# Optimization experiments

Hardware: AMD Instinct MI355X
Metric: run time of the kernel (lower is better)

Reference implementation:

```python
import jax, jax.numpy as jnp
import numpy as np

STRIDE = 4
H, W, A = 208, 336, 3
ANCHOR_SCALE = 8.0
ASPECTS = ((1.0, 1.0), (1.4, 0.7), (0.7, 1.4))  # (aspect_x, aspect_y)
PRE_NMS = 2000
POST_NMS = 1000
IOU_THR = 0.7
BBOX_CLIP = float(np.log(1000.0 / 16.0))


def make_anchors():
    # EfficientDet/SageMakerCV-style anchors at level 2, boxes as (y1, x1, y2, x2)
    base = ANCHOR_SCALE * STRIDE  # 32
    yc = (np.arange(H, dtype=np.float32) + 0.5) * STRIDE
    xc = (np.arange(W, dtype=np.float32) + 0.5) * STRIDE
    yy, xx = np.meshgrid(yc, xc, indexing='ij')  # [H, W]
    per_aspect = []
    for ax, ay in ASPECTS:
        hx, hy = base * ax / 2.0, base * ay / 2.0
        per_aspect.append(np.stack([yy - hy, xx - hx, yy + hy, xx + hx], axis=-1))
    return np.stack(per_aspect, axis=2).reshape(-1, 4).astype(np.float32)  # [H*W*A, 4]


def decode(deltas, anchors):
    # deltas: [B, N, 4] (dy, dx, dh, dw); anchors: [N, 4]; weights (1,1,1,1)
    ah = anchors[:, 2] - anchors[:, 0]
    aw = anchors[:, 3] - anchors[:, 1]
    acy = anchors[:, 0] + 0.5 * ah
    acx = anchors[:, 1] + 0.5 * aw
    dy, dx = deltas[..., 0], deltas[..., 1]
    dh = jnp.clip(deltas[..., 2], -BBOX_CLIP, BBOX_CLIP)
    dw = jnp.clip(deltas[..., 3], -BBOX_CLIP, BBOX_CLIP)
    cy = dy * ah + acy
    cx = dx * aw + acx
    h = jnp.exp(dh) * ah
    w = jnp.exp(dw) * aw
    return jnp.stack([cy - 0.5 * h, cx - 0.5 * w, cy + 0.5 * h, cx + 0.5 * w], axis=-1)


def _iou_one_to_many(box, boxes):
    y1 = jnp.maximum(box[0], boxes[:, 0])
    x1 = jnp.maximum(box[1], boxes[:, 1])
    y2 = jnp.minimum(box[2], boxes[:, 2])
    x2 = jnp.minimum(box[3], boxes[:, 3])
    inter = jnp.maximum(y2 - y1, 0.0) * jnp.maximum(x2 - x1, 0.0)
    a1 = (box[2] - box[0]) * (box[3] - box[1])
    a2 = (boxes[:, 2] - boxes[:, 0]) * (boxes[:, 3] - boxes[:, 1])
    return inter / (a1 + a2 - inter + 1e-8)


def nms_single(boxes, scores):
    # greedy NMS, fixed POST_NMS iterations (jit-friendly)
    def body(i, state):
        sc, kb, ks = state
        j = jnp.argmax(sc)
        b, s = boxes[j], sc[j]
        kb = kb.at[i].set(b)
        ks = ks.at[i].set(s)
        sup = _iou_one_to_many(b, boxes) > IOU_THR  # suppresses j itself (iou=1)
        sc = jnp.where(sup, -1.0, sc)
        return sc, kb, ks

    init = (scores,
            jnp.zeros((POST_NMS, 4), boxes.dtype),
            jnp.zeros((POST_NMS,), scores.dtype))
    _, kb, ks = jax.lax.fori_loop(0, POST_NMS, body, init)
    return kb, ks


def setup_inputs() -> dict:
    key = jax.random.key(0)
    k0, k1, k2 = jax.random.split(key, 3)
    feats = jax.random.normal(k0, (2, H, W, 256), dtype=jnp.float32)
    img_info = jnp.ones((2, 2), jnp.float32) * jnp.array([832.0, 1344.0], jnp.float32)
    w_cls = 0.01 * jax.random.normal(k1, (256, A * 1), dtype=jnp.float32)
    b_cls = jnp.zeros((A * 1,), jnp.float32)
    w_reg = 0.01 * jax.random.normal(k2, (256, A * 4), dtype=jnp.float32)
    b_reg = jnp.zeros((A * 4,), jnp.float32)
    return {"feats": feats, "img_info": img_info, "w_cls": w_cls, "b_cls": b_cls,
            "w_reg": w_reg, "b_reg": b_reg}


def reference(feats, img_info, w_cls, b_cls, w_reg, b_reg):
    B = feats.shape[0]
    # 1x1 convs == channel matmuls
    cls_scores = jnp.einsum('bhwc,co->bhwo', feats, w_cls) + b_cls  # [B,H,W,3]
    bbox_preds = jnp.einsum('bhwc,co->bhwo', feats, w_reg) + b_reg  # [B,H,W,12]

    scores = jax.nn.sigmoid(cls_scores).reshape(B, -1)       # [B, N]
    deltas = bbox_preds.reshape(B, -1, 4)                    # [B, N, 4]
    anchors = jnp.asarray(make_anchors())                    # [N, 4]
    boxes = decode(deltas, anchors)                          # [B, N, 4]

    # clip to image extents
    hmax = img_info[:, 0][:, None]
    wmax = img_info[:, 1][:, None]
    boxes = jnp.stack([
        jnp.clip(boxes[..., 0], 0.0, hmax),
        jnp.clip(boxes[..., 1], 0.0, wmax),
        jnp.clip(boxes[..., 2], 0.0, hmax),
        jnp.clip(boxes[..., 3], 0.0, wmax)], axis=-1)

    # per-image pre-NMS topk
    top_s, idx = jax.lax.top_k(scores, PRE_NMS)              # [B, PRE]
    top_b = jnp.take_along_axis(boxes, idx[..., None], axis=1)  # [B, PRE, 4]

    rois, roi_scores = jax.vmap(nms_single)(top_b, top_s)    # [B, POST, 4], [B, POST]
    return cls_scores, bbox_preds, rois, roi_scores
```

## Files before the change

### kernel.cpp

```cpp
#include <hip/hip_runtime.h>
#include <cstdint>
#include <cstddef>

#define HH 208
#define WW 336
#define NA 3
#define NPER 209664
#define NROWS 139776
#define NB 2
#define PRE_K 2000
#define POST_K 1000
#define CAP 8192
#define MW 32
#define MROWS 2048
#define BBOX_CLIP_F 4.135166556742356f

#define WS_HIST   0
#define WS_HIST2  32768
#define WS_META   65536
#define WS_META24 65544
#define WS_CCNT   65552
#define WS_KEEPW  65568
#define WS_CAND   66080
#define WS_SBOX   197152
#define WS_SSC    261152
#define WS_MASK   277248
#define WS_ZERO_WORDS 49288

__device__ __forceinline__ float sigmoidf_ref(float x) {
  return __fdiv_rn(1.0f, __fadd_rn(1.0f, expf(-x)));
}
__device__ __forceinline__ unsigned int score_u(float logit) {
  float s = sigmoidf_ref(logit);
  return __float_as_uint(s) | 0x80000000u;
}

__device__ __forceinline__ unsigned long long bcast64(unsigned long long v, int l) {
  unsigned int lo = (unsigned int)__builtin_amdgcn_readlane((int)(unsigned int)v, l);
  unsigned int hi = (unsigned int)__builtin_amdgcn_readlane((int)(unsigned int)(v >> 32), l);
  return ((unsigned long long)hi << 32) | lo;
}

__device__ __forceinline__ float4 decode_box(const float* __restrict__ bbox,
                                             int b, unsigned int n,
                                             float hmax, float wmax) {
  unsigned int a = n % 3u;
  unsigned int pix = n / 3u;
  unsigned int y = pix / (unsigned int)WW;
  unsigned int x = pix % (unsigned int)WW;
  float yc = ((float)y + 0.5f) * 4.0f;
  float xc = ((float)x + 0.5f) * 4.0f;
  float hx = (a == 0) ? 16.0f : ((a == 1) ? 22.4f : 11.2f);
  float hy = (a == 0) ? 16.0f : ((a == 1) ? 11.2f : 22.4f);
  float ay1 = __fsub_rn(yc, hy), ax1 = __fsub_rn(xc, hx);
  float ay2 = __fadd_rn(yc, hy), ax2 = __fadd_rn(xc, hx);
  float ah = __fsub_rn(ay2, ay1), aw = __fsub_rn(ax2, ax1);
  float acy = __fadd_rn(ay1, __fmul_rn(0.5f, ah));
  float acx = __fadd_rn(ax1, __fmul_rn(0.5f, aw));
  const float* d = bbox + ((size_t)b * NPER + n) * 4u;
  float dy = d[0], dx = d[1];
  float dh = fminf(fmaxf(d[2], -BBOX_CLIP_F), BBOX_CLIP_F);
  float dw = fminf(fmaxf(d[3], -BBOX_CLIP_F), BBOX_CLIP_F);
  float cy = __fadd_rn(__fmul_rn(dy, ah), acy);
  float cx = __fadd_rn(__fmul_rn(dx, aw), acx);
  float hh = __fmul_rn(expf(dh), ah);
  float wwv = __fmul_rn(expf(dw), aw);
  float y1 = __fsub_rn(cy, __fmul_rn(0.5f, hh));
  float x1 = __fsub_rn(cx, __fmul_rn(0.5f, wwv));
  float y2 = __fadd_rn(cy, __fmul_rn(0.5f, hh));
  float x2 = __fadd_rn(cx, __fmul_rn(0.5f, wwv));
  y1 = fminf(fmaxf(y1, 0.0f), hmax);
  x1 = fminf(fmaxf(x1, 0.0f), wmax);
  y2 = fminf(fmaxf(y2, 0.0f), hmax);
  x2 = fminf(fmaxf(x2, 0.0f), wmax);
  return make_float4(y1, x1, y2, x2);
}

__device__ __forceinline__ float iou_ref(float4 bi, float4 bj) {
  float yA = fmaxf(bi.x, bj.x);
  float xA = fmaxf(bi.y, bj.y);
  float yB = fminf(bi.z, bj.z);
  float xB = fminf(bi.w, bj.w);
  float inter = __fmul_rn(fmaxf(__fsub_rn(yB, yA), 0.0f),
                          fmaxf(__fsub_rn(xB, xA), 0.0f));
  float a1 = __fmul_rn(__fsub_rn(bi.z, bi.x), __fsub_rn(bi.w, bi.y));
  float a2 = __fmul_rn(__fsub_rn(bj.z, bj.x), __fsub_rn(bj.w, bj.y));
  float den = __fadd_rn(__fsub_rn(__fadd_rn(a1, a2), inter), 1e-8f);
  return __fdiv_rn(inter, den);
}

__global__ void k_zero(unsigned int* __restrict__ p, int n) {
  int i = blockIdx.x * blockDim.x + threadIdx.x;
  if (i < n) p[i] = 0u;
}

__global__ __launch_bounds__(256) void k_head(
    const float* __restrict__ feats, const float* __restrict__ w_cls,
    const float* __restrict__ b_cls, const float* __restrict__ w_reg,
    const float* __restrict__ b_reg, float* __restrict__ out_cls,
    float* __restrict__ out_bbox) {
  const int lane = threadIdx.x & 63;
  const int wid = blockIdx.x * (blockDim.x >> 6) + (threadIdx.x >> 6);
  const int nw = gridDim.x * (blockDim.x >> 6);
  const int k0 = lane << 2;
  const int l15 = lane & 15;
  const int ol = ((l15 & 1) << 3) | ((l15 & 2) << 1) | ((l15 & 4) >> 1) |
                 ((l15 & 8) >> 3);

  float wreg[4][16];
#pragma unroll
  for (int j = 0; j < 16; ++j) {
    const int o = ol ^ j;
#pragma unroll
    for (int kk = 0; kk < 4; ++kk) {
      wreg[kk][j] = (o < 3) ? w_cls[(k0 + kk) * 3 + o]
                            : (o < 15 ? w_reg[(k0 + kk) * 12 + (o - 3)] : 0.0f);
    }
  }
  const float bias = (ol < 3) ? b_cls[ol] : (ol < 15 ? b_reg[ol - 3] : 0.0f);

  for (int r = wid; r < NROWS; r += nw) {
    const float4 f4 = *(const float4*)(feats + (size_t)r * 256 + k0);
    float a[16];
#pragma unroll
    for (int j = 0; j < 16; ++j) {
      a[j] = f4.x * wreg[0][j];
      a[j] += f4.y * wreg[1][j];
      a[j] += f4.z * wreg[2][j];
      a[j] += f4.w * wreg[3][j];
    }
#pragma unroll
    for (int s = 0; s < 8; ++s) a[s] += __shfl_xor(a[8 + s], 1, 64);
#pragma unroll
    for (int s = 0; s < 4; ++s) a[s] += __shfl_xor(a[4 + s], 2, 64);
#pragma unroll
    for (int s = 0; s < 2; ++s) a[s] += __shfl_xor(a[2 + s], 4, 64);
    a[0] += __shfl_xor(a[1], 8, 64);
    a[0] += __shfl_xor(a[0], 16, 64);
    a[0] += __shfl_xor(a[0], 32, 64);
    if (lane < 16 && ol < 15) {
      float v = a[0] + bias;
      if (ol < 3) out_cls[(size_t)r * 3 + ol] = v;
      else        out_bbox[(size_t)r * 12 + (ol - 3)] = v;
    }
  }
}

__global__ __launch_bounds__(256) void k_hist(const float* __restrict__ out_cls,
                                              unsigned int* __restrict__ hist) {
  const int b = blockIdx.y;
  __shared__ unsigned int h[4096];
  for (int i = threadIdx.x; i < 4096; i += blockDim.x) h[i] = 0u;
  __syncthreads();
  for (int i = blockIdx.x * blockDim.x + threadIdx.x; i < NPER;
       i += gridDim.x * blockDim.x) {
    unsigned int u = score_u(out_cls[(size_t)b * NPER + i]);
    atomicAdd(&h[u >> 20], 1u);
  }
  __syncthreads();
  for (int i = threadIdx.x; i < 4096; i += blockDim.x)
    if (h[i]) atomicAdd(&hist[b * 4096 + i], h[i]);
}

__global__ __launch_bounds__(1024) void k_thresh(const unsigned int* __restrict__ hist,
                                                 unsigned int* __restrict__ meta_T) {
  const int b = blockIdx.x;
  const int t = threadIdx.x;
  __shared__ unsigned int sums[1024];
  unsigned int hb[4];
  unsigned int s = 0u;
#pragma unroll
  for (int q = 0; q < 4; ++q) {
    int bin = 4095 - (t * 4 + q);
    hb[q] = hist[b * 4096 + bin];
    s += hb[q];
  }
  sums[t] = s;
  __syncthreads();
  for (int off = 1; off < 1024; off <<= 1) {
    unsigned int v = (t >= off) ? sums[t - off] : 0u;
    __syncthreads();
    sums[t] += v;
    __syncthreads();
  }
  unsigned int excl = sums[t] - s;
  if (excl < PRE_K && excl + s >= PRE_K) {
    unsigned int c = excl;
#pragma unroll
    for (int q = 0; q < 4; ++q) {
      c += hb[q];
      if (c >= PRE_K) { meta_T[b] = (unsigned int)(4095 - (t * 4 + q)); break; }
    }
  }
}

__global__ __launch_bounds__(256) void k_hist2(const float* __restrict__ out_cls,
                                               const unsigned int* __restrict__ meta_T,
                                               unsigned int* __restrict__ hist2) {
  const int b = blockIdx.y;
  const unsigned int T = meta_T[b];
  __shared__ unsigned int h[4096];
  for (int i = threadIdx.x; i < 4096; i += blockDim.x) h[i] = 0u;
  __syncthreads();
  for (int i = blockIdx.x * blockDim.x + threadIdx.x; i < NPER;
       i += gridDim.x * blockDim.x) {
    unsigned int u = score_u(out_cls[(size_t)b * NPER + i]);
    if ((u >> 20) == T) atomicAdd(&h[(u >> 8) & 0xFFFu], 1u);
  }
  __syncthreads();
  for (int i = threadIdx.x; i < 4096; i += blockDim.x)
    if (h[i]) atomicAdd(&hist2[b * 4096 + i], h[i]);
}

__global__ __launch_bounds__(1024) void k_thresh2(const unsigned int* __restrict__ hist,
                                                  const unsigned int* __restrict__ hist2,
                                                  const unsigned int* __restrict__ meta_T,
                                                  unsigned int* __restrict__ meta_T24) {
  const int b = blockIdx.x;
  const int t = threadIdx.x;
  const unsigned int T = meta_T[b];
  __shared__ unsigned int sums[1024];
  __shared__ unsigned int c0s;
  unsigned int c0 = 0u;
  for (int i = t; i < 4096; i += 1024)
    if ((unsigned int)i > T) c0 += hist[b * 4096 + i];
  sums[t] = c0;
  __syncthreads();
  for (int off = 512; off > 0; off >>= 1) {
    if (t < off) sums[t] += sums[t + off];
    __syncthreads();
  }
  if (t == 0) c0s = sums[0];
  __syncthreads();
  const unsigned int C0 = c0s;
  __syncthreads();
  unsigned int hb[4];
  unsigned int s = 0u;
#pragma unroll
  for (int q = 0; q < 4; ++q) {
    int bin = 4095 - (t * 4 + q);
    hb[q] = hist2[b * 4096 + bin];
    s += hb[q];
  }
  sums[t] = s;
  __syncthreads();
  for (int off = 1; off < 1024; off <<= 1) {
    unsigned int v = (t >= off) ? sums[t - off] : 0u;
    __syncthreads();
    sums[t] += v;
    __syncthreads();
  }
  unsigned int excl = sums[t] - s;
  if (C0 + excl < PRE_K && C0 + excl + s >= PRE_K) {
    unsigned int c = C0 + excl;
#pragma unroll
    for (int q = 0; q < 4; ++q) {
      c += hb[q];
      if (c >= PRE_K) {
        meta_T24[b] = (T << 12) | (unsigned int)(4095 - (t * 4 + q));
        break;
      }
    }
  }
}

__global__ __launch_bounds__(256) void k_compact(const float* __restrict__ out_cls,
                                                 const unsigned int* __restrict__ meta_T24,
                                                 unsigned int* __restrict__ cand_count,
                                                 unsigned long long* __restrict__ cand) {
  const int b = blockIdx.y;
  const unsigned int T24 = meta_T24[b];
  for (int i = blockIdx.x * blockDim.x + threadIdx.x; i < NPER;
       i += gridDim.x * blockDim.x) {
    unsigned int u = score_u(out_cls[(size_t)b * NPER + i]);
    if ((u >> 8) >= T24) {
      unsigned int pos = atomicAdd(&cand_count[b], 1u);
      if (pos < CAP)
        cand[(size_t)b * CAP + pos] =
            ((unsigned long long)u << 32) | (unsigned int)(~(unsigned int)i);
    }
  }
}

__global__ __launch_bounds__(1024) void k_sort(const unsigned long long* __restrict__ cand,
                                               const unsigned int* __restrict__ cand_count,
                                               const float* __restrict__ out_bbox,
                                               const float* __restrict__ img_info,
                                               float* __restrict__ sboxes,
                                               float* __restrict__ sscores) {
  const int b = blockIdx.x;
  const int t = threadIdx.x;
  __shared__ unsigned long long keys[CAP];
  unsigned int cc = cand_count[b];
  if (cc > CAP) cc = CAP;
  int n = 2048;
  while ((unsigned int)n < cc) n <<= 1;
  for (int i = t; i < n; i += 1024) keys[i] = cand[(size_t)b * CAP + i];
  __syncthreads();
  for (int k = 2; k <= n; k <<= 1) {
    for (int j = k >> 1; j > 0; j >>= 1) {
      for (int i = t; i < n; i += 1024) {
        int ixj = i ^ j;
        if (ixj > i) {
          unsigned long long a = keys[i], c = keys[ixj];
          bool up = ((i & k) == 0);
          bool sw = up ? (a < c) : (a > c);
          if (sw) { keys[i] = c; keys[ixj] = a; }
        }
      }
      __syncthreads();
    }
  }
  const float hmax = img_info[b * 2 + 0];
  const float wmax = img_info[b * 2 + 1];
  for (int i = t; i < PRE_K; i += 1024) {
    unsigned long long key = keys[i];
    unsigned int u = (unsigned int)(key >> 32);
    unsigned int idx = ~(unsigned int)(key & 0xFFFFFFFFull);
    float sc = __uint_as_float(u & 0x7FFFFFFFu);
    float4 bx = decode_box(out_bbox, b, idx, hmax, wmax);
    ((float4*)sboxes)[(size_t)b * PRE_K + i] = bx;
    sscores[(size_t)b * PRE_K + i] = sc;
  }
}

__global__ __launch_bounds__(64) void k_mask(const float* __restrict__ sboxes,
                                             unsigned long long* __restrict__ mask) {
  const int b = blockIdx.z;
  const int rb = blockIdx.x;
  const int cb = blockIdx.y;
  const int t = threadIdx.x;
  __shared__ float4 cbox[64];
  const int col0 = cb * 64;
  {
    int c = col0 + t;
    cbox[t] = (c < PRE_K) ? ((const float4*)sboxes)[(size_t)b * PRE_K + c]
                          : make_float4(0.f, 0.f, 0.f, 0.f);
  }
  __syncthreads();
  const int i = rb * 64 + t;
  if (i >= PRE_K) return;
  float4 bi = ((const float4*)sboxes)[(size_t)b * PRE_K + i];
  unsigned long long bits = 0ull;
#pragma unroll 8
  for (int j = 0; j < 64; ++j) {
    int c = col0 + j;
    if (c > i && c < PRE_K) {
      if (iou_ref(bi, cbox[j]) > 0.7f) bits |= (1ull << j);
    }
  }
  mask[((size_t)b * MROWS + i) * MW + cb] = bits;
}

#define MLOAD(BUF, G)                                                     \
  {                                                                       \
    _Pragma("unroll") for (int _k = 0; _k < 32; ++_k) {                   \
      int _row = (G) * 64 + 2 * _k + psel;                                \
      (BUF)[_k] = (_row < PRE_K) ? M[(size_t)(G) * 2048 + 64 * _k + lane] \
                                 : 0ull;                                  \
    }                                                                     \
  }
#define DLOAD(DST, G)                                                     \
  {                                                                       \
    int _row = (G) * 64 + lane;                                           \
    (DST) = ((G) < 32 && _row < PRE_K) ? M[(size_t)_row * MW + (G)] : 0ull; \
  }
#define GSTEP(G, MCUR, MNEXT, DCUR, DNEXT)                                \
  do {                                                                    \
    MLOAD(MNEXT, (G) + 1);                                                \
    DLOAD(DNEXT, (G) + 1);                                                \
    unsigned long long w = bcast64(remv, (G)) | bcast64(remv, (G) + 32);  \
    unsigned long long alive = ~w;                                        \
    if ((G) == 31) alive &= (1ull << (PRE_K - 31 * 64)) - 1ull;           \
    unsigned long long kept = 0ull;                                       \
    while (alive) {                                                       \
      int j = __builtin_ctzll(alive);                                     \
      unsigned long long bit = 1ull << j;                                 \
      kept |= bit;                                                        \
      unsigned long long dj = bcast64((DCUR), j);                         \
      alive &= ~(dj | bit);                                               \
    }                                                                     \
    int pc = __popcll(kept);                                              \
    if (nk + pc >= POST_K) {                                              \
      int need = POST_K - nk;                                             \
      unsigned long long k2 = kept;                                       \
      for (int _t = 0; _t < need; ++_t) k2 &= k2 - 1;                     \
      kept ^= k2;                \
      if (lane == 0) keepw[b * 32 + (G)] = kept;                          \
      stop = 1;                                                           \
    } else {                                                              \
      nk += pc;                                                           \
      if (lane == 0) keepw[b * 32 + (G)] = kept;                          \
      unsigned long long keptv = kept >> psel;                            \
      _Pragma("unroll") for (int _q = 0; _q < 32; ++_q) {                 \
        unsigned long long sel = 0ull - ((keptv >> (2 * _q)) & 1ull);     \
        remv |= (MCUR)[_q] & sel;                                         \
      }                                                                   \
    }                                                                     \
  } while (0)

__global__ __launch_bounds__(64, 1) void k_scan(
    const unsigned long long* __restrict__ mask,
    unsigned long long* __restrict__ keepw) {
  const int b = blockIdx.x;
  const int lane = threadIdx.x;
  const int psel = lane >> 5;
  const unsigned long long* M = mask + (size_t)b * MROWS * MW;

  unsigned long long mbA[32], mbB[32], dA, dB;
  unsigned long long remv = 0ull;
  int nk = 0, stop = 0;

  MLOAD(mbA, 0);
  DLOAD(dA, 0);
  for (int g = 0; g < 32; g += 2) {
    GSTEP(g, mbA, mbB, dA, dB);
    if (stop) break;
    GSTEP(g + 1, mbB, mbA, dB, dA);
    if (stop) break;
  }
}

__global__ __launch_bounds__(64) void k_write(const float* __restrict__ sboxes,
                                              const float* __restrict__ sscores,
                                              const unsigned long long* __restrict__ keepw,
                                              float* __restrict__ rois,
                                              float* __restrict__ rsc) {
  const int b = blockIdx.x;
  const int lane = threadIdx.x;
  unsigned long long w = (lane < 32) ? keepw[b * 32 + lane] : 0ull;
  int pc = __popcll(w);
  int pref = pc;
#pragma unroll
  for (int off = 1; off < 64; off <<= 1) {
    int v = __shfl_up(pref, off, 64);
    if (lane >= off) pref += v;
  }
  const int excl = pref - pc;
  const int Ktot = __shfl(pref, 63, 64);
  int rank = excl;
  unsigned long long ww = w;
  while (ww) {
    int j = __builtin_ctzll(ww);
    ww &= ww - 1;
    int row = lane * 64 + j;
    ((float4*)rois)[(size_t)b * POST_K + rank] =
        ((const float4*)sboxes)[(size_t)b * PRE_K + row];
    rsc[(size_t)b * POST_K + rank] = sscores[(size_t)b * PRE_K + row];
    ++rank;
  }
  float4 pad = ((const float4*)sboxes)[(size_t)b * PRE_K + 0];
  for (int i = Ktot + lane; i < POST_K; i += 64) {
    ((float4*)rois)[(size_t)b * POST_K + i] = pad;
    rsc[(size_t)b * POST_K + i] = -1.0f;
  }
}

extern "C" void kernel_launch(void* const* d_in, const int* in_sizes, int n_in,
                              void* d_out, int out_size, void* d_ws, size_t ws_size,
                              hipStream_t stream) {
  const float* feats    = (const float*)d_in[0];
  const float* img_info = (const float*)d_in[1];
  const float* w_cls    = (const float*)d_in[2];
  const float* b_cls    = (const float*)d_in[3];
  const float* w_reg    = (const float*)d_in[4];
  const float* b_reg    = (const float*)d_in[5];

  float* out = (float*)d_out;
  float* out_cls  = out;
  float* out_bbox = out + 419328;
  float* out_rois = out + 2096640;
  float* out_rsc  = out + 2104640;

  char* ws = (char*)d_ws;
  unsigned int* hist        = (unsigned int*)(ws + WS_HIST);
  unsigned int* hist2       = (unsigned int*)(ws + WS_HIST2);
  unsigned int* meta_T      = (unsigned int*)(ws + WS_META);
  unsigned int* meta_T24    = (unsigned int*)(ws + WS_META24);
  unsigned int* cand_count  = (unsigned int*)(ws + WS_CCNT);
  unsigned long long* keepw = (unsigned long long*)(ws + WS_KEEPW);
  unsigned long long* cand  = (unsigned long long*)(ws + WS_CAND);
  float* sboxes             = (float*)(ws + WS_SBOX);
  float* sscores            = (float*)(ws + WS_SSC);
  unsigned long long* mask  = (unsigned long long*)(ws + WS_MASK);

  k_zero<<<(WS_ZERO_WORDS + 255) / 256, 256, 0, stream>>>((unsigned int*)ws, WS_ZERO_WORDS);
  k_head<<<2048, 256, 0, stream>>>(feats, w_cls, b_cls, w_reg, b_reg, out_cls, out_bbox);
  k_hist<<<dim3(128, NB), 256, 0, stream>>>(out_cls, hist);
  k_thresh<<<NB, 1024, 0, stream>>>(hist, meta_T);
  k_hist2<<<dim3(128, NB), 256, 0, stream>>>(out_cls, meta_T, hist2);
  k_thresh2<<<NB, 1024, 0, stream>>>(hist, hist2, meta_T, meta_T24);
  k_compact<<<dim3(128, NB), 256, 0, stream>>>(out_cls, meta_T24, cand_count, cand);
  k_sort<<<NB, 1024, 0, stream>>>(cand, cand_count, out_bbox, img_info, sboxes, sscores);
  k_mask<<<dim3(32, 32, NB), 64, 0, stream>>>(sboxes, mask);
  k_scan<<<NB, 64, 0, stream>>>(mask, keepw);
  k_write<<<NB, 64, 0, stream>>>(sboxes, sscores, keepw, out_rois, out_rsc);
}
```

Baseline: 414.0 us.

## Restructure head matmul as row-per-thread with LDS-staged feature tiles

Replaces the one-wave-per-row head kernel, which needed a shuffle reduction per row, with a tiled kernel. Each thread now owns a whole row and accumulates 15 outputs. Features are staged through shared memory in 32-channel chunks, with register prefetch of the next chunk, and the weights are read as uniform scalar loads. This removes the cross-lane shuffle reductions and the mostly idle output lanes, and writes the bbox outputs as float4 stores. In exchange there are more barriers, LDS traffic and register pressure, a grid of only 546 blocks, and a summation order that differs from the old reduction tree.

Result: slower. 449.0 us (+8.5%).

```diff
diff --git a/kernel.cpp b/kernel.cpp
--- a/kernel.cpp
+++ b/kernel.cpp
@@ -94,56 +94,69 @@
   if (i < n) p[i] = 0u;
 }
 
+#define TROWS 256
+#define KCH 32
+#define NCH 8
+#define LSTR 36
+
 __global__ __launch_bounds__(256) void k_head(
     const float* __restrict__ feats, const float* __restrict__ w_cls,
     const float* __restrict__ b_cls, const float* __restrict__ w_reg,
     const float* __restrict__ b_reg, float* __restrict__ out_cls,
     float* __restrict__ out_bbox) {
-  const int lane = threadIdx.x & 63;
-  const int wid = blockIdx.x * (blockDim.x >> 6) + (threadIdx.x >> 6);
-  const int nw = gridDim.x * (blockDim.x >> 6);
-  const int k0 = lane << 2;
-  const int l15 = lane & 15;
-  const int ol = ((l15 & 1) << 3) | ((l15 & 2) << 1) | ((l15 & 4) >> 1) |
-                 ((l15 & 8) >> 3);
-
-  float wreg[4][16];
-#pragma unroll
-  for (int j = 0; j < 16; ++j) {
-    const int o = ol ^ j;
-#pragma unroll
-    for (int kk = 0; kk < 4; ++kk) {
-      wreg[kk][j] = (o < 3) ? w_cls[(k0 + kk) * 3 + o]
-                            : (o < 15 ? w_reg[(k0 + kk) * 12 + (o - 3)] : 0.0f);
-    }
-  }
-  const float bias = (ol < 3) ? b_cls[ol] : (ol < 15 ? b_reg[ol - 3] : 0.0f);
-
-  for (int r = wid; r < NROWS; r += nw) {
-    const float4 f4 = *(const float4*)(feats + (size_t)r * 256 + k0);
-    float a[16];
-#pragma unroll
-    for (int j = 0; j < 16; ++j) {
-      a[j] = f4.x * wreg[0][j];
-      a[j] += f4.y * wreg[1][j];
-      a[j] += f4.z * wreg[2][j];
-      a[j] += f4.w * wreg[3][j];
-    }
-#pragma unroll
-    for (int s = 0; s < 8; ++s) a[s] += __shfl_xor(a[8 + s], 1, 64);
-#pragma unroll
-    for (int s = 0; s < 4; ++s) a[s] += __shfl_xor(a[4 + s], 2, 64);
-#pragma unroll
-    for (int s = 0; s < 2; ++s) a[s] += __shfl_xor(a[2 + s], 4, 64);
-    a[0] += __shfl_xor(a[1], 8, 64);
-    a[0] += __shfl_xor(a[0], 16, 64);
-    a[0] += __shfl_xor(a[0], 32, 64);
-    if (lane < 16 && ol < 15) {
-      float v = a[0] + bias;
-      if (ol < 3) out_cls[(size_t)r * 3 + ol] = v;
-      else        out_bbox[(size_t)r * 12 + (ol - 3)] = v;
-    }
-  }
+  __shared__ float lds[TROWS * LSTR];
+  const int t = threadIdx.x;
+  const int r0 = blockIdx.x * TROWS;
+  const int sr = t >> 3;
+  const int sc = t & 7;
+
+  float acc[15];
+#pragma unroll
+  for (int o = 0; o < 15; ++o) acc[o] = 0.0f;
+
+  float4 stg[8];
+#pragma unroll
+  for (int j = 0; j < 8; ++j)
+    stg[j] = *(const float4*)(feats + (size_t)(r0 + sr + j * 32) * 256 + sc * 4);
+
+  for (int c = 0; c < NCH; ++c) {
+    __syncthreads();
+#pragma unroll
+    for (int j = 0; j < 8; ++j)
+      *(float4*)&lds[(sr + j * 32) * LSTR + sc * 4] = stg[j];
+    __syncthreads();
+    if (c + 1 < NCH) {
+      const int cn = (c + 1) * KCH;
+#pragma unroll
+      for (int j = 0; j < 8; ++j)
+        stg[j] = *(const float4*)(feats + (size_t)(r0 + sr + j * 32) * 256 + cn + sc * 4);
+    }
+    const int kg0 = c * KCH;
+#pragma unroll
+    for (int kk = 0; kk < 8; ++kk) {
+      const float4 xv = *(const float4*)&lds[t * LSTR + kk * 4];
+      const float xq[4] = {xv.x, xv.y, xv.z, xv.w};
+#pragma unroll
+      for (int q = 0; q < 4; ++q) {
+        const int kg = kg0 + kk * 4 + q;
+        const float* wcp = w_cls + kg * 3;
+        const float* wrp = w_reg + kg * 12;
+        acc[0] += xq[q] * wcp[0];
+        acc[1] += xq[q] * wcp[1];
+        acc[2] += xq[q] * wcp[2];
+#pragma unroll
+        for (int o = 0; o < 12; ++o) acc[3 + o] += xq[q] * wrp[o];
+      }
+    }
+  }
+  const size_t row = (size_t)(r0 + t);
+  out_cls[row * 3 + 0] = acc[0] + b_cls[0];
+  out_cls[row * 3 + 1] = acc[1] + b_cls[1];
+  out_cls[row * 3 + 2] = acc[2] + b_cls[2];
+  float4* ob = (float4*)(out_bbox + row * 12);
+  ob[0] = make_float4(acc[3] + b_reg[0], acc[4] + b_reg[1], acc[5] + b_reg[2], acc[6] + b_reg[3]);
+  ob[1] = make_float4(acc[7] + b_reg[4], acc[8] + b_reg[5], acc[9] + b_reg[6], acc[10] + b_reg[7]);
+  ob[2] = make_float4(acc[11] + b_reg[8], acc[12] + b_reg[9], acc[13] + b_reg[10], acc[14] + b_reg[11]);
 }
 
 __global__ __launch_bounds__(256) void k_hist(const float* __restrict__ out_cls,
@@ -485,7 +498,7 @@
   unsigned long long* mask  = (unsigned long long*)(ws + WS_MASK);
 
   k_zero<<<(WS_ZERO_WORDS + 255) / 256, 256, 0, stream>>>((unsigned int*)ws, WS_ZERO_WORDS);
-  k_head<<<2048, 256, 0, stream>>>(feats, w_cls, b_cls, w_reg, b_reg, out_cls, out_bbox);
+  k_head<<<NROWS / TROWS, 256, 0, stream>>>(feats, w_cls, b_cls, w_reg, b_reg, out_cls, out_bbox);
   k_hist<<<dim3(128, NB), 256, 0, stream>>>(out_cls, hist);
   k_thresh<<<NB, 1024, 0, stream>>>(hist, meta_T);
   k_hist2<<<dim3(128, NB), 256, 0, stream>>>(out_cls, meta_T, hist2);
```
